# Kernel tuning notes

Measured on AMD Instinct MI355X. Metric: run time of the kernel, lower is better.

Reference implementation:

```python
import jax, jax.numpy as jnp
import numpy as np

# Dims: B=batch, H=query heads, HKV=kv heads, T=query len, S=cache/key len, Dh=head dim
B, H, HKV, T, S, Dh = 2, 32, 8, 1024, 2048, 128
THRESH = 0.000488  # keep keys whose mean attention (over heads and queries) exceeds this


def setup_inputs() -> dict:
    key = jax.random.key(0)
    k1, k2, k3 = jax.random.split(key, 3)
    # attn_w emulates post-softmax attention probabilities: rows sum to 1 over key axis
    attn_w = jax.random.uniform(k1, (B, H, T, S), dtype=jnp.float32)
    attn_w = attn_w / attn_w.sum(axis=-1, keepdims=True)
    v = jax.random.normal(k2, (B, HKV, S, Dh), dtype=jnp.float32)
    w_o = jax.random.normal(k3, (H * Dh, H * Dh), dtype=jnp.float32) * 0.02  # o_proj weight (no bias, Mistral)
    return {"attn_w": attn_w, "v": v, "w_o": w_o}


def reference(attn_w, v, w_o):
    # keep = attn_w.mean(dim=(1,2)) > thresh  -> [B, S]
    keep = attn_w.mean(axis=(1, 2)) > THRESH
    pruned_weights = attn_w * keep[:, None, None, :].astype(attn_w.dtype)  # [B,H,T,S]
    # repeat_kv: [B,HKV,S,Dh] -> [B,H,S,Dh] via repeat_interleave on head axis
    groups = attn_w.shape[1] // v.shape[1]
    v_full = jnp.repeat(v, groups, axis=1)
    new_ctx = jnp.einsum('bhts,bhsd->bhtd', pruned_weights, v_full)  # [B,H,T,Dh]
    Bn, Hn, Tn, Dn = new_ctx.shape
    new_ctx = new_ctx.transpose(0, 2, 1, 3).reshape(Bn, Tn, Hn * Dn)  # [B,T,H*Dh]
    out = new_ctx @ w_o.T  # o_proj
    return (out, pruned_weights)
```

## Files before the change

kernel.cpp:

```cpp
#include <hip/hip_runtime.h>
#include <hip/hip_bf16.h>

#define B_ 2
#define H_ 32
#define HKV_ 8
#define T_ 1024
#define S_ 2048
#define DH_ 128
#define HD_ 4096
#define NROW_ 32768
#define THRESH_D 0.000488

typedef __attribute__((ext_vector_type(4))) float f32x4;
typedef __attribute__((ext_vector_type(8))) short bf16x8;

#define SCHED0() __builtin_amdgcn_sched_barrier(0)

__device__ __forceinline__ void gload_lds16(const void* g, void* l) {
  __builtin_amdgcn_global_load_lds(
      (const __attribute__((address_space(1))) void*)g,
      (__attribute__((address_space(3))) void*)l, 16, 0, 0);
}

__global__ void colsum_partial_k(const float* __restrict__ attn,
                                 double* __restrict__ partial) {
  int tid = threadIdx.x;
  int b = blockIdx.z, y = blockIdx.y;
  int s = blockIdx.x * 1024 + tid * 4;
  const float* base = attn + (size_t)(b * NROW_ + y * 128) * S_ + s;
  double a0 = 0.0, a1 = 0.0, a2 = 0.0, a3 = 0.0;
  for (int r = 0; r < 128; ++r) {
    float4 vv = *(const float4*)(base + (size_t)r * S_);
    a0 += vv.x; a1 += vv.y; a2 += vv.z; a3 += vv.w;
  }
  double* o = partial + (size_t)(b * 256 + y) * S_ + s;
  o[0] = a0; o[1] = a1; o[2] = a2; o[3] = a3;
}

__global__ void reduce_keep_k(const double* __restrict__ partial,
                              float* __restrict__ keep) {
  __shared__ double sh[4][64];
  int b = blockIdx.x >> 5;
  int s0 = (blockIdx.x & 31) * 64;
  int w = threadIdx.x >> 6, l = threadIdx.x & 63;
  const double* p = partial + (size_t)b * 256 * S_ + s0 + l;
  double sum = 0.0;
  #pragma unroll 8
  for (int y = 0; y < 64; ++y) sum += p[(size_t)(w * 64 + y) * S_];
  sh[w][l] = sum;
  __syncthreads();
  if (w == 0) {
    double t = (sh[0][l] + sh[1][l]) + (sh[2][l] + sh[3][l]);
    keep[b * S_ + s0 + l] = (t * (1.0 / 32768.0) > THRESH_D) ? 1.0f : 0.0f;
  }
}

__global__ void convert_v_k(const float* __restrict__ v,
                            __hip_bfloat16* __restrict__ vt) {
  __shared__ float tile[32][33];
  int bh = blockIdx.z;
  int s0 = blockIdx.x * 32, d0 = blockIdx.y * 32;
  const float* vp = v + (size_t)bh * (S_ * DH_);
  __hip_bfloat16* vtp = vt + (size_t)bh * (S_ * DH_);
  int tx = threadIdx.x, ty = threadIdx.y;
  for (int i = 0; i < 32; i += 8)
    tile[ty + i][tx] = vp[(size_t)(s0 + ty + i) * DH_ + d0 + tx];
  __syncthreads();
  int s = s0 + tx;
  for (int i = 0; i < 32; i += 8) {
    int d = d0 + ty + i;
    int ssw = (s & ~63) | ((s ^ ((d & 7) << 3)) & 63);
    vtp[(size_t)d * S_ + ssw] = __float2bfloat16(tile[tx][ty + i]);
  }
}

__global__ void convert_wo_k(const float* __restrict__ w,
                             __hip_bfloat16* __restrict__ wb) {
  size_t idx = ((size_t)blockIdx.x * 256 + threadIdx.x) * 8;
  int n = (int)(idx >> 12);
  int k0 = (int)(idx & (HD_ - 1));
  float4 x = *(const float4*)(w + idx);
  float4 y = *(const float4*)(w + idx + 4);
  union { bf16x8 v8; __hip_bfloat16 h[8]; } u;
  u.h[0] = __float2bfloat16(x.x); u.h[1] = __float2bfloat16(x.y);
  u.h[2] = __float2bfloat16(x.z); u.h[3] = __float2bfloat16(x.w);
  u.h[4] = __float2bfloat16(y.x); u.h[5] = __float2bfloat16(y.y);
  u.h[6] = __float2bfloat16(y.z); u.h[7] = __float2bfloat16(y.w);
  int ksw = (k0 & ~63) | ((k0 ^ ((n & 7) << 3)) & 63);
  *(bf16x8*)(wb + (size_t)n * HD_ + ksw) = u.v8;
}

#define BK1 64
#define NS1 32

__global__ __launch_bounds__(512, 4) void prune_gemm1_k(
    const float* __restrict__ attn, const float* __restrict__ keep,
    const __hip_bfloat16* __restrict__ vt, float* __restrict__ pruned,
    __hip_bfloat16* __restrict__ ctx) {
  __shared__ __align__(16) __hip_bfloat16 As[2][128 * BK1];
  __shared__ __align__(16) __hip_bfloat16 Bs[2][128 * BK1];
  __shared__ float ksh[S_];

  int tid = threadIdx.x;
  int lg = ((blockIdx.x & 7) << 6) | (blockIdx.x >> 3);
  int bh = lg >> 3;
  int t0 = (lg & 7) * 128;
  int b = bh >> 5, h = bh & 31, hkv = h >> 2;
  const float* A = attn + ((size_t)bh * T_ + t0) * S_;
  float* P = pruned + ((size_t)bh * T_ + t0) * S_;
  const __hip_bfloat16* Bv = vt + (size_t)(b * HKV_ + hkv) * (DH_ * S_);
  const float* kp = keep + b * S_;

  int arow = tid >> 2;
  int acol = (tid & 3) * 16;
  int wave = tid >> 6, lane = tid & 63;
  int l16 = lane & 15, lk = lane >> 4;

  f32x4 acc[8];
  f32x4 z = {0.f, 0.f, 0.f, 0.f};
  #pragma unroll
  for (int n = 0; n < 8; ++n) acc[n] = z;

  float4 areg[4];

  {
    int i4 = tid * 4;
    *(float4*)&ksh[i4] = *(const float4*)(kp + i4);
  }

  auto issueA = [&](int ks) {
    const float* ga = A + (size_t)arow * S_ + ks * BK1 + acol;
    #pragma unroll
    for (int j = 0; j < 4; ++j) areg[j] = *(const float4*)(ga + j * 4);
  };

  auto issueB = [&](int ks, int buf) {
    const __hip_bfloat16* g0 = Bv + (size_t)(tid >> 3) * S_ + ks * BK1 + (tid & 7) * 8;
    char* lb = (char*)&Bs[buf][0] + tid * 16;
    gload_lds16(g0, lb);
    gload_lds16(g0 + (size_t)64 * S_, lb + 8192);
  };

  auto stageA = [&](int ks, int buf) {
    float4 p[4];
    #pragma unroll
    for (int j = 0; j < 4; ++j) {
      float4 kv = *(const float4*)&ksh[ks * BK1 + acol + j * 4];
      p[j].x = areg[j].x * kv.x;
      p[j].y = areg[j].y * kv.y;
      p[j].z = areg[j].z * kv.z;
      p[j].w = areg[j].w * kv.w;
    }
    float* gp = P + (size_t)arow * S_ + ks * BK1 + acol;
    #pragma unroll
    for (int j = 0; j < 4; ++j) *(float4*)(gp + j * 4) = p[j];
    union { bf16x8 v8; __hip_bfloat16 h[8]; } u0, u1;
    const float* pf = (const float*)&p[0];
    #pragma unroll
    for (int j = 0; j < 8; ++j) u0.h[j] = __float2bfloat16(pf[j]);
    #pragma unroll
    for (int j = 0; j < 8; ++j) u1.h[j] = __float2bfloat16(pf[8 + j]);
    char* ab = (char*)&As[buf][0];
    int base0 = arow * 128 + acol * 2;
    int sw = (arow & 7) << 4;
    *(bf16x8*)(ab + (base0 ^ sw)) = u0.v8;
    *(bf16x8*)(ab + ((base0 + 16) ^ sw)) = u1.v8;
  };

  auto mfmaStep = [&](int buf) {
    char* ab = (char*)&As[buf][0];
    char* bb = (char*)&Bs[buf][0];
    #pragma unroll
    for (int kk = 0; kk < 2; ++kk) {
      int kb = kk * 64 + lk * 16;
      int ar = wave * 16 + l16;
      bf16x8 af = *(const bf16x8*)(ab + (ar * 128 + (kb ^ ((ar & 7) << 4))));
      #pragma unroll
      for (int n = 0; n < 8; ++n) {
        int br = n * 16 + l16;
        bf16x8 bf = *(const bf16x8*)(bb + (br * 128 + (kb ^ ((br & 7) << 4))));
        acc[n] = __builtin_amdgcn_mfma_f32_16x16x32_bf16(af, bf, acc[n], 0, 0, 0);
      }
    }
  };

  issueA(0);
  issueB(0, 0);
  SCHED0();
  asm volatile("s_waitcnt lgkmcnt(0)" ::: "memory");
  SCHED0();
  __builtin_amdgcn_s_barrier();
  SCHED0();
  stageA(0, 0);
  issueA(1);
  SCHED0();
  asm volatile("s_waitcnt vmcnt(8) lgkmcnt(0)" ::: "memory");
  SCHED0();
  __builtin_amdgcn_s_barrier();
  SCHED0();

  for (int ks = 0; ks < NS1; ++ks) {
    int cur = ks & 1;
    if (ks + 1 < NS1) issueB(ks + 1, cur ^ 1);
    SCHED0();
    if (ks + 1 < NS1) stageA(ks + 1, cur ^ 1);
    if (ks + 2 < NS1) issueA(ks + 2);
    mfmaStep(cur);
    SCHED0();
    asm volatile("s_waitcnt vmcnt(8) lgkmcnt(0)" ::: "memory");
    SCHED0();
    __builtin_amdgcn_s_barrier();
    SCHED0();
  }

  #pragma unroll
  for (int n = 0; n < 8; ++n)
    #pragma unroll
    for (int r = 0; r < 4; ++r) {
      int trow = t0 + wave * 16 + lk * 4 + r;
      int rowm = b * T_ + trow;
      int kcol = h * DH_ + n * 16 + l16;
      int ksw = (kcol & ~63) | ((kcol ^ ((rowm & 7) << 3)) & 63);
      ctx[(size_t)rowm * HD_ + ksw] = __float2bfloat16(acc[n][r]);
    }
}

#define BK2 64
#define NS2 64

__global__ __launch_bounds__(512) void gemm2_k(
    const __hip_bfloat16* __restrict__ Actx,
    const __hip_bfloat16* __restrict__ Bw,
    float* __restrict__ out) {
  __shared__ __align__(16) __hip_bfloat16 As[2][128 * BK2];
  __shared__ __align__(16) __hip_bfloat16 Bs[2][128 * BK2];
  int tid = threadIdx.x;
  int lg = ((blockIdx.x & 7) << 6) | (blockIdx.x >> 3);
  int n0 = (lg >> 4) * 128;
  int m0 = (lg & 15) * 128;
  const __hip_bfloat16* Ap = Actx + (size_t)m0 * HD_;
  const __hip_bfloat16* Bp = Bw + (size_t)n0 * HD_;
  int wave = tid >> 6, lane = tid & 63;
  int l16 = lane & 15, lk = lane >> 4;

  f32x4 acc[8];
  f32x4 z = {0.f, 0.f, 0.f, 0.f};
  #pragma unroll
  for (int n = 0; n < 8; ++n) acc[n] = z;

  auto issue = [&](int ks, int buf) {
    const __hip_bfloat16* ga = Ap + (size_t)(tid >> 3) * HD_ + ks * BK2 + (tid & 7) * 8;
    const __hip_bfloat16* gb = Bp + (size_t)(tid >> 3) * HD_ + ks * BK2 + (tid & 7) * 8;
    char* la = (char*)&As[buf][0] + tid * 16;
    char* lb = (char*)&Bs[buf][0] + tid * 16;
    gload_lds16(ga, la);
    gload_lds16(ga + (size_t)64 * HD_, la + 8192);
    gload_lds16(gb, lb);
    gload_lds16(gb + (size_t)64 * HD_, lb + 8192);
  };

  auto mfmaStep = [&](int buf) {
    char* ab = (char*)&As[buf][0];
    char* bb = (char*)&Bs[buf][0];
    #pragma unroll
    for (int kk = 0; kk < 2; ++kk) {
      int kb = kk * 64 + lk * 16;
      int ar = wave * 16 + l16;
      bf16x8 af = *(const bf16x8*)(ab + (ar * 128 + (kb ^ ((ar & 7) << 4))));
      #pragma unroll
      for (int n = 0; n < 8; ++n) {
        int br = n * 16 + l16;
        bf16x8 bf = *(const bf16x8*)(bb + (br * 128 + (kb ^ ((br & 7) << 4))));
        acc[n] = __builtin_amdgcn_mfma_f32_16x16x32_bf16(af, bf, acc[n], 0, 0, 0);
      }
    }
  };

  issue(0, 0);
  __syncthreads();
  for (int ks = 0; ks < NS2; ++ks) {
    int cur = ks & 1;
    if (ks + 1 < NS2) issue(ks + 1, cur ^ 1);
    mfmaStep(cur);
    __syncthreads();
  }

  #pragma unroll
  for (int n = 0; n < 8; ++n)
    #pragma unroll
    for (int r = 0; r < 4; ++r) {
      int row = m0 + wave * 16 + lk * 4 + r;
      int col = n0 + n * 16 + l16;
      out[(size_t)row * HD_ + col] = acc[n][r];
    }
}

extern "C" void kernel_launch(void* const* d_in, const int* in_sizes, int n_in,
                              void* d_out, int out_size, void* d_ws, size_t ws_size,
                              hipStream_t stream) {
  const float* attn = (const float*)d_in[0];
  const float* v = (const float*)d_in[1];
  const float* w_o = (const float*)d_in[2];
  float* out = (float*)d_out;
  float* pruned = out + (size_t)B_ * T_ * HD_;

  char* ws = (char*)d_ws;
  size_t off = 0;
  double* partial = (double*)(ws + off); off += (size_t)B_ * 256 * S_ * 8;
  float* keep = (float*)(ws + off);      off += (size_t)B_ * S_ * 4;
  __hip_bfloat16* vt = (__hip_bfloat16*)(ws + off);
  off += (size_t)B_ * HKV_ * DH_ * S_ * 2;
  __hip_bfloat16* wo = (__hip_bfloat16*)(ws + off);
  off += (size_t)HD_ * HD_ * 2;
  __hip_bfloat16* ctx = (__hip_bfloat16*)(ws + off);
  off += (size_t)B_ * T_ * HD_ * 2;

  colsum_partial_k<<<dim3(2, 256, B_), 256, 0, stream>>>(attn, partial);
  reduce_keep_k<<<dim3(64), 256, 0, stream>>>(partial, keep);
  convert_v_k<<<dim3(S_ / 32, DH_ / 32, B_ * HKV_), dim3(32, 8), 0, stream>>>(v, vt);
  convert_wo_k<<<dim3((HD_ * HD_) / (256 * 8)), 256, 0, stream>>>(w_o, wo);
  prune_gemm1_k<<<dim3(512), 512, 0, stream>>>(attn, keep, vt, pruned, ctx);
  gemm2_k<<<dim3(512), 512, 0, stream>>>(ctx, wo, out);

  (void)in_sizes; (void)n_in; (void)out_size; (void)ws_size;
}
```

Measured before the change: 542.4 us.

## Rework pipeline waits in fused prune-GEMM and o_proj GEMM, async keep load

```diff
diff --git a/kernel.cpp b/kernel.cpp
--- a/kernel.cpp
+++ b/kernel.cpp
@@ -22,15 +22,15 @@
       (__attribute__((address_space(3))) void*)l, 16, 0, 0);
 }
 
-__global__ void colsum_partial_k(const float* __restrict__ attn,
-                                 double* __restrict__ partial) {
+__global__ __launch_bounds__(256) void colsum_partial_k(
+    const float* __restrict__ attn, double* __restrict__ partial) {
   int tid = threadIdx.x;
   int b = blockIdx.z, y = blockIdx.y;
   int s = blockIdx.x * 1024 + tid * 4;
   const float* base = attn + (size_t)(b * NROW_ + y * 128) * S_ + s;
   double a0 = 0.0, a1 = 0.0, a2 = 0.0, a3 = 0.0;
   for (int r = 0; r < 128; ++r) {
-    float4 vv = *(const float4*)(base + (size_t)r * S_);
+    f32x4 vv = *(const f32x4*)(base + (size_t)r * S_);
     a0 += vv.x; a1 += vv.y; a2 += vv.z; a3 += vv.w;
   }
   double* o = partial + (size_t)(b * 256 + y) * S_ + s;
@@ -99,7 +99,7 @@
     __hip_bfloat16* __restrict__ ctx) {
   __shared__ __align__(16) __hip_bfloat16 As[2][128 * BK1];
   __shared__ __align__(16) __hip_bfloat16 Bs[2][128 * BK1];
-  __shared__ float ksh[S_];
+  __shared__ __align__(16) float ksh[S_];
 
   int tid = threadIdx.x;
   int lg = ((blockIdx.x & 7) << 6) | (blockIdx.x >> 3);
@@ -121,17 +121,12 @@
   #pragma unroll
   for (int n = 0; n < 8; ++n) acc[n] = z;
 
-  float4 areg[4];
-
-  {
-    int i4 = tid * 4;
-    *(float4*)&ksh[i4] = *(const float4*)(kp + i4);
-  }
+  f32x4 areg[4];
 
   auto issueA = [&](int ks) {
     const float* ga = A + (size_t)arow * S_ + ks * BK1 + acol;
     #pragma unroll
-    for (int j = 0; j < 4; ++j) areg[j] = *(const float4*)(ga + j * 4);
+    for (int j = 0; j < 4; ++j) areg[j] = *(const f32x4*)(ga + j * 4);
   };
 
   auto issueB = [&](int ks, int buf) {
@@ -142,18 +137,16 @@
   };
 
   auto stageA = [&](int ks, int buf) {
-    float4 p[4];
+    f32x4 p[4];
     #pragma unroll
     for (int j = 0; j < 4; ++j) {
-      float4 kv = *(const float4*)&ksh[ks * BK1 + acol + j * 4];
-      p[j].x = areg[j].x * kv.x;
-      p[j].y = areg[j].y * kv.y;
-      p[j].z = areg[j].z * kv.z;
-      p[j].w = areg[j].w * kv.w;
+      f32x4 kv = *(const f32x4*)&ksh[ks * BK1 + acol + j * 4];
+      p[j] = areg[j] * kv;
     }
     float* gp = P + (size_t)arow * S_ + ks * BK1 + acol;
     #pragma unroll
-    for (int j = 0; j < 4; ++j) *(float4*)(gp + j * 4) = p[j];
+    for (int j = 0; j < 4; ++j)
+      __builtin_nontemporal_store(p[j], (f32x4*)(gp + j * 4));
     union { bf16x8 v8; __hip_bfloat16 h[8]; } u0, u1;
     const float* pf = (const float*)&p[0];
     #pragma unroll
@@ -184,30 +177,34 @@
     }
   };
 
+  gload_lds16(kp + tid * 4, (char*)ksh + tid * 16);
+  issueB(0, 0);
   issueA(0);
-  issueB(0, 0);
   SCHED0();
-  asm volatile("s_waitcnt lgkmcnt(0)" ::: "memory");
+  asm volatile("s_waitcnt vmcnt(6)" ::: "memory");
   SCHED0();
   __builtin_amdgcn_s_barrier();
   SCHED0();
   stageA(0, 0);
   issueA(1);
-  SCHED0();
-  asm volatile("s_waitcnt vmcnt(8) lgkmcnt(0)" ::: "memory");
-  SCHED0();
-  __builtin_amdgcn_s_barrier();
-  SCHED0();
 
   for (int ks = 0; ks < NS1; ++ks) {
     int cur = ks & 1;
-    if (ks + 1 < NS1) issueB(ks + 1, cur ^ 1);
-    SCHED0();
-    if (ks + 1 < NS1) stageA(ks + 1, cur ^ 1);
+    if (ks + 1 < NS1) {
+      issueB(ks + 1, cur ^ 1);
+      stageA(ks + 1, cur ^ 1);
+    }
     if (ks + 2 < NS1) issueA(ks + 2);
+    SCHED0();
+    if (ks + 2 < NS1) {
+      asm volatile("s_waitcnt vmcnt(10) lgkmcnt(0)" ::: "memory");
+    } else {
+      asm volatile("s_waitcnt vmcnt(4) lgkmcnt(0)" ::: "memory");
+    }
+    SCHED0();
+    __builtin_amdgcn_s_barrier();
+    SCHED0();
     mfmaStep(cur);
-    SCHED0();
-    asm volatile("s_waitcnt vmcnt(8) lgkmcnt(0)" ::: "memory");
     SCHED0();
     __builtin_amdgcn_s_barrier();
     SCHED0();
@@ -277,12 +274,22 @@
   };
 
   issue(0, 0);
-  __syncthreads();
   for (int ks = 0; ks < NS2; ++ks) {
     int cur = ks & 1;
     if (ks + 1 < NS2) issue(ks + 1, cur ^ 1);
+    SCHED0();
+    if (ks + 1 < NS2) {
+      asm volatile("s_waitcnt vmcnt(4) lgkmcnt(0)" ::: "memory");
+    } else {
+      asm volatile("s_waitcnt vmcnt(0) lgkmcnt(0)" ::: "memory");
+    }
+    SCHED0();
+    __builtin_amdgcn_s_barrier();
+    SCHED0();
     mfmaStep(cur);
-    __syncthreads();
+    SCHED0();
+    __builtin_amdgcn_s_barrier();
+    SCHED0();
   }
 
   #pragma unroll
```

Measured after the change: 851.9 us. 57.1% more time.
